# Kernel optimization log

Hardware: AMD Instinct MI355X
Metric: run time of the kernel (lower is better)

Reference implementation:

```python
import jax, jax.numpy as jnp
import numpy as np

V, D, T, B, MS, WIN, EOS = 10000, 256, 128, 8, 4, 1, 4
S = MS + 1          # decoder segment length (y_input0 + MAX_SEGMENT tokens)
HRATE = 0.1
LOGINF = 1e6


def setup_inputs() -> dict:
    key = jax.random.key(0)
    ks = jax.random.split(key, 17)
    s = lambda i, shape: (jax.random.normal(ks[i], shape, jnp.float32) * 0.05)
    return dict(
        x_ids=jax.random.randint(ks[0], (B, T + 2 * WIN), 0, V),
        lens=jnp.full((B,), T, dtype=jnp.int32),
        emb=s(1, (V, D)),
        y_start=s(2, (1, D)),
        cell_Wi=s(3, (4 * D, D)), cell_Wh=s(4, (4 * D, D)), cell_b=s(5, (4 * D,)),
        yin0_W=s(6, (D, D)), yin0_b=s(7, (D,)),
        hlin_W=s(8, (2 * D, D)), hlin_b=s(9, (2 * D,)),
        l0_Wi=s(10, (4 * D, D)), l0_Wh=s(11, (4 * D, D)), l0_b=s(12, (4 * D,)),
        l1_Wi=s(13, (4 * D, D)), l1_Wh=s(14, (4 * D, D)), l1_b=s(15, (4 * D,)),
        out_b=s(16, (V,)),
    )


def _cell(x, h, c, Wi, Wh, b):
    # torch LSTM gate order: i, f, g, o
    g = x @ Wi.T + h @ Wh.T + b
    i, f, gg, o = jnp.split(g, 4, axis=-1)
    c2 = jax.nn.sigmoid(f) * c + jax.nn.sigmoid(i) * jnp.tanh(gg)
    return jax.nn.sigmoid(o) * jnp.tanh(c2), c2


def reference(x_ids, lens, emb, y_start, cell_Wi, cell_Wh, cell_b,
              yin0_W, yin0_b, hlin_W, hlin_b,
              l0_Wi, l0_Wh, l0_b, l1_Wi, l1_Wh, l1_b, out_b):
    y = x_ids[:, WIN:-WIN]                     # [B, T] target ids
    x = emb[y]                                 # [B, T, D]

    # --- encoder LSTMCell scan over j_start (state persists across schedule) ---
    seq = jnp.concatenate(
        [jnp.broadcast_to(y_start, (B, D))[None], jnp.transpose(x, (1, 0, 2))[:-1]], 0)  # [T,B,D]
    z = jnp.zeros((B, D), x.dtype)
    def enc_step(carry, xt):
        h, c = carry
        h2, c2 = _cell(xt, h, c, cell_Wi, cell_Wh, cell_b)
        return (h2, c2), h2
    _, h_seq = jax.lax.scan(enc_step, (z, z), seq)        # [T, B, D]

    drop_h = HRATE * h_seq
    y_in0 = drop_h @ yin0_W.T + yin0_b                    # [T, B, D]
    h0_all = jnp.tanh(drop_h @ hlin_W.T + hlin_b).reshape(T, B, 2, D)  # per-layer init h

    # --- build decoder inputs [T, B, S, D]: (y_input0, x[j_start:j_start+MS]) ---
    xp = jnp.pad(x, ((0, 0), (0, MS), (0, 0)))            # zero-pad time (causal => pads don't affect valid outputs)
    pos = jnp.arange(T)[:, None] + jnp.arange(MS)[None, :]           # [T, MS]
    seg_x = jnp.transpose(xp[:, pos], (1, 0, 2, 3))       # [T, B, MS, D]
    seg = jnp.concatenate([y_in0[:, :, None, :], seg_x], axis=2)     # [T, B, S, D]

    # --- 2-layer LSTM decoder, vmapped over j_start ---
    def decode(seg_t, h_init):                            # seg_t [B,S,D], h_init [B,2,D]
        def step(carry, xt):
            (h0, c0), (h1, c1) = carry
            h0n, c0n = _cell(xt, h0, c0, l0_Wi, l0_Wh, l0_b)
            h1n, c1n = _cell(h0n, h1, c1, l1_Wi, l1_Wh, l1_b)
            return ((h0n, c0n), (h1n, c1n)), h1n
        init = ((h_init[:, 0], z), (h_init[:, 1], z))
        _, hs = jax.lax.scan(step, init, jnp.transpose(seg_t, (1, 0, 2)))
        return jnp.transpose(hs, (1, 0, 2))               # [B, S, D]
    dec_h = jax.vmap(decode)(seg, h0_all)                 # [T, B, S, D]

    # --- tied output projection + log-softmax (only needed gathers kept) ---
    logits = jnp.einsum('tbsd,vd->tbsv', dec_h, emb) + out_b         # [T,B,S,V]
    logZ = jax.nn.logsumexp(logits, axis=-1)                          # [T,B,S]

    tgt = jnp.transpose(y[:, jnp.clip(pos, 0, T - 1)], (1, 0, 2))     # [T,B,MS]
    tgt_lp = jnp.take_along_axis(logits[:, :, :MS, :], tgt[..., None], axis=3)[..., 0] \
             - logZ[:, :, :MS]                                        # [T,B,MS]
    pmask = (pos < T)[:, None, :]
    cum = jnp.cumsum(jnp.where(pmask, tgt_lp, 0.0), axis=2)           # [T,B,MS]
    eos_lp = logits[:, :, 1:, EOS] - logZ[:, :, 1:]                   # [T,B,MS]

    kmask = (jnp.arange(T)[:, None] + jnp.arange(1, MS + 1)[None, :]) <= T   # [T,MS]
    body = jnp.where(kmask[:, None, :], cum + eos_lp, -LOGINF)        # [T,B,MS]
    logpy = jnp.concatenate([jnp.full((T, 1, B), -LOGINF, body.dtype),
                             jnp.transpose(body, (0, 2, 1))], axis=1)  # [T, MS+1, B]

    # --- alpha forward DP: alpha[j] = logsumexp_L alpha[j-L] + logpy[j-L][L] ---
    jj = jnp.arange(1, T + 1)[:, None]
    ii = jnp.arange(MS)[None, :]
    sstart = jj - MS + ii                                             # [T,MS]
    LPG = jnp.where((sstart >= 0)[..., None],
                    logpy[jnp.clip(sstart, 0), jnp.broadcast_to(MS - ii, (T, MS))],
                    -LOGINF)                                          # [T,MS,B]

    Apad0 = jnp.full((MS + T + 1, B), -LOGINF, logpy.dtype).at[MS].set(0.0)
    def dp_step(Apad, args):
        j, lpg = args
        win = jax.lax.dynamic_slice(Apad, (j, 0), (MS, B))            # alpha[j-MS .. j-1]
        aj = jax.nn.logsumexp(win + lpg, axis=0)
        return jax.lax.dynamic_update_slice(Apad, aj[None], (MS + j, 0)), None
    Apad, _ = jax.lax.scan(dp_step, Apad0, (jnp.arange(1, T + 1), LPG))
    alpha = Apad[MS:]                                                 # [T+1, B]

    ret = -jnp.sum(alpha[lens, jnp.arange(B)]) / jnp.sum(lens).astype(alpha.dtype)
    return ret
```

## Files before the change

kernel.cpp:

```cpp
#include <hip/hip_runtime.h>

#define V_ 10000
#define D_ 256
#define T_ 128
#define B_ 8
#define MS_ 4
#define S_ 5
#define EOS_ 4

typedef unsigned short b16_t;
typedef __attribute__((ext_vector_type(8))) short s16x8;
typedef __attribute__((ext_vector_type(8))) unsigned short u16x8;
typedef __attribute__((ext_vector_type(4))) float f32x4;
typedef __attribute__((ext_vector_type(2))) _Float16 h16x2;

__device__ inline b16_t f2bf(float f) {
  union { float f; unsigned u; } v; v.f = f;
  unsigned r = v.u + 0x7FFFu + ((v.u >> 16) & 1u);
  return (b16_t)(r >> 16);
}
__device__ inline float bf2f(b16_t h) {
  union { unsigned u; float f; } v; v.u = ((unsigned)h) << 16; return v.f;
}
__device__ inline float sigm_(float x) { return 1.0f / (1.0f + __expf(-x)); }
__device__ inline float tanh_(float x) { return 2.0f / (1.0f + __expf(-2.0f * x)) - 1.0f; }
__device__ inline h16x2 bch(unsigned u) { return __builtin_bit_cast(h16x2, u); }
__device__ inline unsigned pkh(float a, float b) {
  h16x2 v; v.x = (_Float16)a; v.y = (_Float16)b;
  return __builtin_bit_cast(unsigned, v);
}

#if __has_builtin(__builtin_amdgcn_fdot2)
#define FDOT2(a, b, c) __builtin_amdgcn_fdot2((a), (b), (c), false)
#else
#define FDOT2(a, b, c) ((c) + (float)(a).x * (float)(b).x + (float)(a).y * (float)(b).y)
#endif

__device__ inline float qswap1(float x) {
  return __builtin_bit_cast(float, __builtin_amdgcn_update_dpp(
      0, __builtin_bit_cast(int, x), 0xB1, 0xF, 0xF, true));
}
__device__ inline float qswap2(float x) {
  return __builtin_bit_cast(float, __builtin_amdgcn_update_dpp(
      0, __builtin_bit_cast(int, x), 0x4E, 0xF, 0xF, true));
}

__device__ inline void cvt4(const float* __restrict__ s, b16_t* __restrict__ d) {
  float4 v = *(const float4*)s;
  ushort4 o = { f2bf(v.x), f2bf(v.y), f2bf(v.z), f2bf(v.w) };
  *(ushort4*)d = o;
}

__global__ void k_prep(const float* __restrict__ emb, const float* __restrict__ cWi,
                       const float* __restrict__ y0W, const float* __restrict__ hlW,
                       const float* __restrict__ l0Wi, const float* __restrict__ l0Wh,
                       const float* __restrict__ l1Wi, const float* __restrict__ l1Wh,
                       const float* __restrict__ cWh, const int* __restrict__ x_ids,
                       const float* __restrict__ y_st,
                       b16_t* __restrict__ emb_bf, b16_t* __restrict__ cWi_bf,
                       b16_t* __restrict__ y0W_bf, b16_t* __restrict__ hlW_bf,
                       b16_t* __restrict__ l0Wi_bf, b16_t* __restrict__ l0Wh_bf,
                       b16_t* __restrict__ Wcat_bf, unsigned* __restrict__ Whf,
                       b16_t* __restrict__ seq_bf, b16_t* __restrict__ seg_bf) {
  for (long i = (long)blockIdx.x * blockDim.x + threadIdx.x; i < 1410048L;
       i += (long)gridDim.x * blockDim.x) {
    if (i < 640000L) { cvt4(emb + i * 4, emb_bf + i * 4); }
    else if (i < 705536L) { long j = i - 640000L; cvt4(cWi + j * 4, cWi_bf + j * 4); }
    else if (i < 721920L) { long j = i - 705536L; cvt4(y0W + j * 4, y0W_bf + j * 4); }
    else if (i < 754688L) { long j = i - 721920L; cvt4(hlW + j * 4, hlW_bf + j * 4); }
    else if (i < 820224L) { long j = i - 754688L; cvt4(l0Wi + j * 4, l0Wi_bf + j * 4); }
    else if (i < 885760L) { long j = i - 820224L; cvt4(l0Wh + j * 4, l0Wh_bf + j * 4); }
    else if (i < 1016832L) {
      long j = (i - 885760L) * 4;
      long n = j >> 9; int k = (int)(j & 511);
      const float* src = (k < 256) ? (l1Wi + n * 256 + k) : (l1Wh + n * 256 + (k - 256));
      cvt4(src, Wcat_bf + j);
    } else if (i < 1082368L) {
      long j = i - 1016832L;
      float4 v = *(const float4*)(cWh + j * 4);
      Whf[2 * j] = pkh(v.x, v.y);
      Whf[2 * j + 1] = pkh(v.z, v.w);
    } else if (i < 1147904L) {
      long j = i - 1082368L;
      int m = (int)(j >> 6), c = (int)(j & 63) * 4;
      int t = m >> 3, b = m & 7;
      const float* src = (t == 0) ? (y_st + c)
                                  : (emb + (size_t)x_ids[b * (T_ + 2) + t] * D_ + c);
      cvt4(src, seq_bf + (size_t)m * D_ + c);
    } else {
      long j = i - 1147904L;
      int r = (int)(j >> 6), c = (int)(j & 63) * 4;
      int p = r >> 2, s = 1 + (r & 3);
      int t = p >> 3, b = p & 7;
      int tt = t + s - 1;
      int ps = r + (r >> 2) + 1;
      if (tt < T_) {
        int tok = x_ids[b * (T_ + 2) + tt + 1];
        cvt4(emb + (size_t)tok * D_ + c, seg_bf + (size_t)ps * 256 + c);
      } else {
        ushort4 z = {0, 0, 0, 0};
        *(ushort4*)(seg_bf + (size_t)ps * 256 + c) = z;
      }
    }
  }
}

__global__ __launch_bounds__(256) void k_gemm(const b16_t* __restrict__ A, int lda,
                                              const b16_t* __restrict__ Bw,
                                              const float* __restrict__ bias,
                                              float* __restrict__ C, int ldc) {
  __shared__ b16_t As[64][264];
  __shared__ b16_t Bs[64][264];
  int tid = threadIdx.x;
  int rowBase = blockIdx.x * 64, colBase = blockIdx.y * 64;
  for (int i = tid; i < 64 * 32; i += 256) {
    int r = i >> 5, c = (i & 31) * 8;
    *(u16x8*)&As[r][c] = *(const u16x8*)(A + (size_t)(rowBase + r) * lda + c);
    *(u16x8*)&Bs[r][c] = *(const u16x8*)(Bw + (size_t)(colBase + r) * 256 + c);
  }
  __syncthreads();
  int w = tid >> 6, l = tid & 63, lr = l & 15, kg = l >> 4;
  f32x4 acc[4] = {{0.f,0.f,0.f,0.f},{0.f,0.f,0.f,0.f},{0.f,0.f,0.f,0.f},{0.f,0.f,0.f,0.f}};
  f32x4 acc2[4] = {{0.f,0.f,0.f,0.f},{0.f,0.f,0.f,0.f},{0.f,0.f,0.f,0.f},{0.f,0.f,0.f,0.f}};
  for (int kk = 0; kk < 4; ++kk) {
    s16x8 a = *(const s16x8*)&As[w * 16 + lr][kk * 32 + kg * 8];
    s16x8 a2 = *(const s16x8*)&As[w * 16 + lr][(kk + 4) * 32 + kg * 8];
#pragma unroll
    for (int f = 0; f < 4; ++f) {
      s16x8 b = *(const s16x8*)&Bs[f * 16 + lr][kk * 32 + kg * 8];
      s16x8 b2 = *(const s16x8*)&Bs[f * 16 + lr][(kk + 4) * 32 + kg * 8];
      acc[f] = __builtin_amdgcn_mfma_f32_16x16x32_bf16(a, b, acc[f], 0, 0, 0);
      acc2[f] = __builtin_amdgcn_mfma_f32_16x16x32_bf16(a2, b2, acc2[f], 0, 0, 0);
    }
  }
#pragma unroll
  for (int f = 0; f < 4; ++f) {
#pragma unroll
    for (int r = 0; r < 4; ++r) {
      int m = rowBase + w * 16 + kg * 4 + r;
      int n = colBase + f * 16 + lr;
      C[(size_t)m * ldc + n] = acc[f][r] + acc2[f][r] + bias[n];
    }
  }
}

#define ENC_Q4(i0)                                                             \
  do {                                                                         \
    uint4 a0 = hp[i0], a1 = hp[i0 + 1], a2 = hp[i0 + 2], a3 = hp[i0 + 3];      \
    s0 = FDOT2(bch(a0.x), bch(wv[4 * (i0) + 0]), s0);                          \
    s1 = FDOT2(bch(a0.x), bch(wv[32 + 4 * (i0) + 0]), s1);                     \
    s0 = FDOT2(bch(a0.y), bch(wv[4 * (i0) + 1]), s0);                          \
    s1 = FDOT2(bch(a0.y), bch(wv[32 + 4 * (i0) + 1]), s1);                     \
    s0 = FDOT2(bch(a0.z), bch(wv[4 * (i0) + 2]), s0);                          \
    s1 = FDOT2(bch(a0.z), bch(wv[32 + 4 * (i0) + 2]), s1);                     \
    s0 = FDOT2(bch(a0.w), bch(wv[4 * (i0) + 3]), s0);                          \
    s1 = FDOT2(bch(a0.w), bch(wv[32 + 4 * (i0) + 3]), s1);                     \
    s0 = FDOT2(bch(a1.x), bch(wv[4 * (i0) + 4]), s0);                          \
    s1 = FDOT2(bch(a1.x), bch(wv[32 + 4 * (i0) + 4]), s1);                     \
    s0 = FDOT2(bch(a1.y), bch(wv[4 * (i0) + 5]), s0);                          \
    s1 = FDOT2(bch(a1.y), bch(wv[32 + 4 * (i0) + 5]), s1);                     \
    s0 = FDOT2(bch(a1.z), bch(wv[4 * (i0) + 6]), s0);                          \
    s1 = FDOT2(bch(a1.z), bch(wv[32 + 4 * (i0) + 6]), s1);                     \
    s0 = FDOT2(bch(a1.w), bch(wv[4 * (i0) + 7]), s0);                          \
    s1 = FDOT2(bch(a1.w), bch(wv[32 + 4 * (i0) + 7]), s1);                     \
    s0 = FDOT2(bch(a2.x), bch(wv[4 * (i0) + 8]), s0);                          \
    s1 = FDOT2(bch(a2.x), bch(wv[32 + 4 * (i0) + 8]), s1);                     \
    s0 = FDOT2(bch(a2.y), bch(wv[4 * (i0) + 9]), s0);                          \
    s1 = FDOT2(bch(a2.y), bch(wv[32 + 4 * (i0) + 9]), s1);                     \
    s0 = FDOT2(bch(a2.z), bch(wv[4 * (i0) + 10]), s0);                         \
    s1 = FDOT2(bch(a2.z), bch(wv[32 + 4 * (i0) + 10]), s1);                    \
    s0 = FDOT2(bch(a2.w), bch(wv[4 * (i0) + 11]), s0);                         \
    s1 = FDOT2(bch(a2.w), bch(wv[32 + 4 * (i0) + 11]), s1);                    \
    s0 = FDOT2(bch(a3.x), bch(wv[4 * (i0) + 12]), s0);                         \
    s1 = FDOT2(bch(a3.x), bch(wv[32 + 4 * (i0) + 12]), s1);                    \
    s0 = FDOT2(bch(a3.y), bch(wv[4 * (i0) + 13]), s0);                         \
    s1 = FDOT2(bch(a3.y), bch(wv[32 + 4 * (i0) + 13]), s1);                    \
    s0 = FDOT2(bch(a3.z), bch(wv[4 * (i0) + 14]), s0);                         \
    s1 = FDOT2(bch(a3.z), bch(wv[32 + 4 * (i0) + 14]), s1);                    \
    s0 = FDOT2(bch(a3.w), bch(wv[4 * (i0) + 15]), s0);                         \
    s1 = FDOT2(bch(a3.w), bch(wv[32 + 4 * (i0) + 15]), s1);                    \
  } while (0)

struct EncS { unsigned hbuf[144]; float gl[256]; };
struct GemS { b16_t As[64][264]; b16_t Bs[64][264]; };

__global__ __launch_bounds__(512, 2) void k_enc_x0(
    const unsigned* __restrict__ Whf,
    const float* __restrict__ encX,
    unsigned* __restrict__ hglob,
    b16_t* __restrict__ droph,
    const b16_t* __restrict__ seg_bf, const b16_t* __restrict__ l0Wi_bf,
    const float* __restrict__ l0b, float* __restrict__ X0) {
  __shared__ union { EncS e; GemS g; } sm;
  int tid = threadIdx.x;
  if (blockIdx.x < 32) {
    int b = blockIdx.x & 7, q = blockIdx.x >> 3;
    int rp = tid >> 2, cq = tid & 3;
    int r0l = 2 * rp;
    int grow0 = ((r0l >> 6) << 8) + q * 64 + (r0l & 63);
    unsigned wv[64];
    {
      const uint4* wp0 = (const uint4*)(Whf + (size_t)grow0 * 128 + cq * 32);
      const uint4* wp1 = (const uint4*)(Whf + (size_t)(grow0 + 1) * 128 + cq * 32);
#pragma unroll
      for (int i = 0; i < 8; ++i) {
        uint4 v = wp0[i];
        wv[4*i] = v.x; wv[4*i+1] = v.y; wv[4*i+2] = v.z; wv[4*i+3] = v.w;
      }
#pragma unroll
      for (int i = 0; i < 8; ++i) {
        uint4 v = wp1[i];
        wv[32+4*i] = v.x; wv[32+4*i+1] = v.y; wv[32+4*i+2] = v.z; wv[32+4*i+3] = v.w;
      }
    }
#pragma unroll
    for (int i = 0; i < 64; ++i) asm volatile("" : "+v"(wv[i]));
    if (tid < 144) sm.e.hbuf[tid] = 0;
    float c = 0.f;
    float ex = encX[(size_t)b * 1024 + grow0 + (cq & 1)];
    __syncthreads();
#pragma unroll 1
    for (int t = 0; t < 128; ++t) {
      const uint4* hp = (const uint4*)&sm.e.hbuf[cq * 36];
      float s0 = 0.f, s1 = 0.f;
      ENC_Q4(0);
      __builtin_amdgcn_sched_barrier(0);
      ENC_Q4(4);
      s0 += qswap1(s0); s0 += qswap2(s0);
      s1 += qswap1(s1); s1 += qswap2(s1);
      if (cq == 0) sm.e.gl[r0l] = s0 + ex;
      else if (cq == 1) sm.e.gl[r0l + 1] = s1 + ex;
      __syncthreads();
      if (tid < 64) {
        float gi = sm.e.gl[tid], gf = sm.e.gl[64 + tid];
        float gg = sm.e.gl[128 + tid], go = sm.e.gl[192 + tid];
        float c2 = sigm_(gf) * c + sigm_(gi) * tanh_(gg);
        float h2 = sigm_(go) * tanh_(c2);
        c = c2;
        float hnb = qswap1(h2);
        if ((tid & 1) == 0) {
          unsigned pk = pkh(h2, hnb) | 0x00010001u;
          sm.e.hbuf[q * 36 + (tid >> 1)] = pk;
          if (t < 127)
            __hip_atomic_store(&hglob[(((size_t)t * 8 + b) * 4 + q) * 32 + (tid >> 1)],
                               pk, __ATOMIC_RELAXED, __HIP_MEMORY_SCOPE_AGENT);
        }
        droph[((size_t)t * 8 + b) * 256 + q * 64 + tid] = f2bf(0.1f * h2);
      }
      if (t < 127) {
        if (tid >= 64 && tid < 160) {
          int idx = tid - 64;
          int ro = idx >> 5;
          int rq = ro + (ro >= q);
          int dw = idx & 31;
          unsigned* src = &hglob[(((size_t)t * 8 + b) * 4 + rq) * 32 + dw];
          unsigned v;
          do {
            v = __hip_atomic_load(src, __ATOMIC_RELAXED, __HIP_MEMORY_SCOPE_AGENT);
          } while (v == 0u);
          sm.e.hbuf[rq * 36 + dw] = v;
        }
        ex = encX[((size_t)(t + 1) * 8 + b) * 1024 + grow0 + (cq & 1)];
        __syncthreads();
      }
    }
  } else {
    int bx2 = blockIdx.x - 32;
    int rb = (bx2 & 63) * 64;
    int colBase = (bx2 >> 6) * 64;
    if (tid < 256) {
      for (int i = tid; i < 64 * 32; i += 256) {
        int r = i >> 5, cc = (i & 31) * 8;
        int jj = rb + r, ps = jj + (jj >> 2) + 1;
        *(u16x8*)&sm.g.As[r][cc] = *(const u16x8*)(seg_bf + (size_t)ps * 256 + cc);
        *(u16x8*)&sm.g.Bs[r][cc] = *(const u16x8*)(l0Wi_bf + (size_t)(colBase + r) * 256 + cc);
      }
    }
    __syncthreads();
    if (tid < 256) {
      int w = tid >> 6, l = tid & 63, lr = l & 15, kg = l >> 4;
      f32x4 acc[4] = {{0.f,0.f,0.f,0.f},{0.f,0.f,0.f,0.f},{0.f,0.f,0.f,0.f},{0.f,0.f,0.f,0.f}};
      f32x4 acc2[4] = {{0.f,0.f,0.f,0.f},{0.f,0.f,0.f,0.f},{0.f,0.f,0.f,0.f},{0.f,0.f,0.f,0.f}};
      for (int kk = 0; kk < 4; ++kk) {
        s16x8 a = *(const s16x8*)&sm.g.As[w * 16 + lr][kk * 32 + kg * 8];
        s16x8 a2 = *(const s16x8*)&sm.g.As[w * 16 + lr][(kk + 4) * 32 + kg * 8];
#pragma unroll
        for (int f = 0; f < 4; ++f) {
          s16x8 b = *(const s16x8*)&sm.g.Bs[f * 16 + lr][kk * 32 + kg * 8];
          s16x8 b2 = *(const s16x8*)&sm.g.Bs[f * 16 + lr][(kk + 4) * 32 + kg * 8];
          acc[f] = __builtin_amdgcn_mfma_f32_16x16x32_bf16(a, b, acc[f], 0, 0, 0);
          acc2[f] = __builtin_amdgcn_mfma_f32_16x16x32_bf16(a2, b2, acc2[f], 0, 0, 0);
        }
      }
#pragma unroll
      for (int f = 0; f < 4; ++f) {
#pragma unroll
        for (int r = 0; r < 4; ++r) {
          int jj = rb + w * 16 + kg * 4 + r;
          int ps = jj + (jj >> 2) + 1;
          int n = colBase + f * 16 + lr;
          X0[(size_t)ps * 1024 + n] = acc[f][r] + acc2[f][r] + l0b[n];
        }
      }
    }
  }
}

__global__ __launch_bounds__(256) void k_proj(
    const b16_t* __restrict__ droph, const b16_t* __restrict__ y0W_bf,
    const float* __restrict__ y0b, const b16_t* __restrict__ hlW_bf,
    const float* __restrict__ hlb, b16_t* __restrict__ seg_bf,
    b16_t* __restrict__ hcat,
    const b16_t* __restrict__ l0Wi_bf, const float* __restrict__ l0b,
    float* __restrict__ X0) {
  __shared__ b16_t As[64][264];
  __shared__ b16_t Bs[64][264];
  int bx = blockIdx.x, by = blockIdx.y;
  const b16_t* Ab; int lda;
  const b16_t* Bw; const float* bias; int colBase, mode;
  if (by < 4)       { Ab = droph;  lda = 256;  Bw = y0W_bf;  bias = y0b; colBase = by * 64;        mode = 0; }
  else if (by < 12) { Ab = droph;  lda = 256;  Bw = hlW_bf;  bias = hlb; colBase = (by - 4) * 64;  mode = 1; }
  else              { Ab = seg_bf; lda = 1280; Bw = l0Wi_bf; bias = l0b; colBase = (by - 12) * 64; mode = 2; }
  int rowBase = bx * 64;
  int tid = threadIdx.x;
  for (int i = tid; i < 64 * 32; i += 256) {
    int r = i >> 5, c = (i & 31) * 8;
    *(u16x8*)&As[r][c] = *(const u16x8*)(Ab + (size_t)(rowBase + r) * lda + c);
    *(u16x8*)&Bs[r][c] = *(const u16x8*)(Bw + (size_t)(colBase + r) * 256 + c);
  }
  __syncthreads();
  int w = tid >> 6, l = tid & 63, lr = l & 15, kg = l >> 4;
  f32x4 acc[4] = {{0.f,0.f,0.f,0.f},{0.f,0.f,0.f,0.f},{0.f,0.f,0.f,0.f},{0.f,0.f,0.f,0.f}};
  f32x4 acc2[4] = {{0.f,0.f,0.f,0.f},{0.f,0.f,0.f,0.f},{0.f,0.f,0.f,0.f},{0.f,0.f,0.f,0.f}};
  for (int kk = 0; kk < 4; ++kk) {
    s16x8 a = *(const s16x8*)&As[w * 16 + lr][kk * 32 + kg * 8];
    s16x8 a2 = *(const s16x8*)&As[w * 16 + lr][(kk + 4) * 32 + kg * 8];
#pragma unroll
    for (int f = 0; f < 4; ++f) {
      s16x8 b = *(const s16x8*)&Bs[f * 16 + lr][kk * 32 + kg * 8];
      s16x8 b2 = *(const s16x8*)&Bs[f * 16 + lr][(kk + 4) * 32 + kg * 8];
      acc[f] = __builtin_amdgcn_mfma_f32_16x16x32_bf16(a, b, acc[f], 0, 0, 0);
      acc2[f] = __builtin_amdgcn_mfma_f32_16x16x32_bf16(a2, b2, acc2[f], 0, 0, 0);
    }
  }
#pragma unroll
  for (int f = 0; f < 4; ++f) {
#pragma unroll
    for (int r = 0; r < 4; ++r) {
      int m = rowBase + w * 16 + kg * 4 + r;
      int n = colBase + f * 16 + lr;
      float v = acc[f][r] + acc2[f][r] + bias[n];
      if (mode == 0) seg_bf[(size_t)m * 1280 + n] = f2bf(v);
      else if (mode == 1) hcat[(size_t)m * 512 + n] = f2bf(tanh_(v));
      else X0[(size_t)m * 5120 + n] = v;
    }
  }
}

__global__ __launch_bounds__(512) void k_dec2(
    b16_t* __restrict__ hcat,
    const b16_t* __restrict__ l0Wh_bf,
    const b16_t* __restrict__ Wcat_bf,
    const float* __restrict__ X0,
    const float* __restrict__ l1b,
    float* __restrict__ c0, float* __restrict__ c1,
    b16_t* __restrict__ dec_out, int s) {
  __shared__ b16_t A0s[16][264];
  __shared__ b16_t A1s[16][520];
  int tid = threadIdx.x;
  int R0 = blockIdx.x * 16;
  for (int i = tid; i < 16 * 32; i += 512) {
    int r = i >> 5, cc = (i & 31) * 8;
    *(u16x8*)&A0s[r][cc] = *(const u16x8*)(hcat + (size_t)(R0 + r) * 512 + cc);
    *(u16x8*)&A1s[r][256 + cc] = *(const u16x8*)(hcat + (size_t)(R0 + r) * 512 + 256 + cc);
  }
  __syncthreads();
  int w = tid >> 6, l = tid & 63, lr = l & 15, kg = l >> 4;
  {
    s16x8 af[8];
#pragma unroll
    for (int kk = 0; kk < 8; ++kk)
      af[kk] = *(const s16x8*)&A0s[lr][kk * 32 + kg * 8];
    f32x4 acc[4][2];
#pragma unroll
    for (int g = 0; g < 4; ++g)
#pragma unroll
      for (int ct = 0; ct < 2; ++ct) acc[g][ct] = f32x4{0.f, 0.f, 0.f, 0.f};
#pragma unroll
    for (int g = 0; g < 4; ++g)
#pragma unroll
      for (int ct = 0; ct < 2; ++ct) {
        int n = g * 256 + w * 32 + ct * 16 + lr;
        const b16_t* bp = l0Wh_bf + (size_t)n * 256 + kg * 8;
#pragma unroll
        for (int kk = 0; kk < 8; ++kk)
          acc[g][ct] = __builtin_amdgcn_mfma_f32_16x16x32_bf16(
              af[kk], *(const s16x8*)(bp + kk * 32), acc[g][ct], 0, 0, 0);
      }
#pragma unroll
    for (int ct = 0; ct < 2; ++ct)
#pragma unroll
      for (int r = 0; r < 4; ++r) {
        int row = kg * 4 + r, p = R0 + row, d = w * 32 + ct * 16 + lr;
        const float* xp = X0 + ((size_t)p * 5 + s) * 1024;
        float gi = acc[0][ct][r] + xp[d],       gf = acc[1][ct][r] + xp[256 + d];
        float gg = acc[2][ct][r] + xp[512 + d], go = acc[3][ct][r] + xp[768 + d];
        float cc0 = c0[(size_t)p * 256 + d];
        float c2 = sigm_(gf) * cc0 + sigm_(gi) * tanh_(gg);
        float h2 = sigm_(go) * tanh_(c2);
        c0[(size_t)p * 256 + d] = c2;
        b16_t hb = f2bf(h2);
        A1s[row][d] = hb;
        hcat[(size_t)p * 512 + d] = hb;
      }
  }
  __syncthreads();
  {
    s16x8 a1[16];
#pragma unroll
    for (int kk = 0; kk < 16; ++kk)
      a1[kk] = *(const s16x8*)&A1s[lr][kk * 32 + kg * 8];
    f32x4 acc[4][2];
#pragma unroll
    for (int g = 0; g < 4; ++g)
#pragma unroll
      for (int ct = 0; ct < 2; ++ct) acc[g][ct] = f32x4{0.f, 0.f, 0.f, 0.f};
#pragma unroll
    for (int g = 0; g < 4; ++g)
#pragma unroll
      for (int ct = 0; ct < 2; ++ct) {
        int n = g * 256 + w * 32 + ct * 16 + lr;
        const b16_t* bp = Wcat_bf + (size_t)n * 512 + kg * 8;
#pragma unroll
        for (int kk = 0; kk < 16; ++kk)
          acc[g][ct] = __builtin_amdgcn_mfma_f32_16x16x32_bf16(
              a1[kk], *(const s16x8*)(bp + kk * 32), acc[g][ct], 0, 0, 0);
      }
#pragma unroll
    for (int ct = 0; ct < 2; ++ct)
#pragma unroll
      for (int r = 0; r < 4; ++r) {
        int row = kg * 4 + r, p = R0 + row, d = w * 32 + ct * 16 + lr;
        float gi = acc[0][ct][r] + l1b[d],       gf = acc[1][ct][r] + l1b[256 + d];
        float gg = acc[2][ct][r] + l1b[512 + d], go = acc[3][ct][r] + l1b[768 + d];
        float cc1 = c1[(size_t)p * 256 + d];
        float c2 = sigm_(gf) * cc1 + sigm_(gi) * tanh_(gg);
        float h2 = sigm_(go) * tanh_(c2);
        c1[(size_t)p * 256 + d] = c2;
        b16_t hb = f2bf(h2);
        hcat[(size_t)p * 512 + 256 + d] = hb;
        dec_out[((size_t)p * 5 + s) * 256 + d] = hb;
      }
  }
}

__global__ __launch_bounds__(512) void k_logits_ext(
    const b16_t* __restrict__ Abf, const b16_t* __restrict__ emb_bf,
    const float* __restrict__ out_b, float* __restrict__ sumexp,
    const int* __restrict__ x_ids, float* __restrict__ tl,
    float* __restrict__ el) {
  int bid = blockIdx.x;
  int tid = threadIdx.x;
  if (bid < 560) {
    __shared__ b16_t Bs[64][264];
    int rowBase = (bid % 40) * 128;
    int w = tid >> 6, l = tid & 63, lr = l & 15, kg = l >> 4;
    s16x8 af[8];
    {
      const b16_t* arow = Abf + (size_t)(rowBase + w * 16 + lr) * 256;
#pragma unroll
      for (int kk = 0; kk < 8; ++kk) af[kk] = *(const s16x8*)(arow + kk * 32 + kg * 8);
    }
    float runsum[4] = {0.f, 0.f, 0.f, 0.f};
    int t0 = (bid / 40) * 12, t1 = (t0 + 12 < 157) ? (t0 + 12) : 157;
    for (int tile = t0; tile < t1; ++tile) {
      int colBase = tile * 64;
      __syncthreads();
      for (int i = tid; i < 64 * 32; i += 512) {
        int r = i >> 5, cc = (i & 31) * 8;
        int vrow = colBase + r;
        u16x8 bv = {0, 0, 0, 0, 0, 0, 0, 0};
        if (vrow < V_) bv = *(const u16x8*)(emb_bf + (size_t)vrow * D_ + cc);
        *(u16x8*)&Bs[r][cc] = bv;
      }
      __syncthreads();
      f32x4 acc[4] = {{0.f,0.f,0.f,0.f},{0.f,0.f,0.f,0.f},{0.f,0.f,0.f,0.f},{0.f,0.f,0.f,0.f}};
      f32x4 acc2[4] = {{0.f,0.f,0.f,0.f},{0.f,0.f,0.f,0.f},{0.f,0.f,0.f,0.f},{0.f,0.f,0.f,0.f}};
#pragma unroll
      for (int kk = 0; kk < 4; ++kk) {
#pragma unroll
        for (int f = 0; f < 4; ++f) {
          s16x8 b = *(const s16x8*)&Bs[f * 16 + lr][kk * 32 + kg * 8];
          s16x8 b2 = *(const s16x8*)&Bs[f * 16 + lr][(kk + 4) * 32 + kg * 8];
          acc[f] = __builtin_amdgcn_mfma_f32_16x16x32_bf16(af[kk], b, acc[f], 0, 0, 0);
          acc2[f] = __builtin_amdgcn_mfma_f32_16x16x32_bf16(af[kk + 4], b2, acc2[f], 0, 0, 0);
        }
      }
#pragma unroll
      for (int f = 0; f < 4; ++f) {
        int n = colBase + f * 16 + lr;
        if (n < V_) {
          float ob = out_b[n];
#pragma unroll
          for (int r = 0; r < 4; ++r) runsum[r] += __expf(acc[f][r] + acc2[f][r] + ob);
        }
      }
    }
#pragma unroll
    for (int r = 0; r < 4; ++r) {
      float rs = runsum[r];
      rs += __shfl_xor(rs, 1, 64);
      rs += __shfl_xor(rs, 2, 64);
      rs += __shfl_xor(rs, 4, 64);
      rs += __shfl_xor(rs, 8, 64);
      if (lr == 0) atomicAdd(&sumexp[rowBase + w * 16 + kg * 4 + r], rs);
    }
  } else {
    int p = (bid - 560) * 8 + (tid >> 6);
    int lane = tid & 63;
    int t = p >> 3, b = p & 7;
    for (int s = 0; s < S_; ++s) {
      const b16_t* hr = Abf + ((size_t)p * S_ + s) * D_;
      float hv[4];
#pragma unroll
      for (int j = 0; j < 4; ++j) hv[j] = bf2f(hr[lane * 4 + j]);
      if (s < MS_) {
        int pos = t + s; if (pos > T_ - 1) pos = T_ - 1;
        int tok = x_ids[b * (T_ + 2) + pos + 1];
        const b16_t* er = emb_bf + (size_t)tok * D_;
        float ps = 0.f;
#pragma unroll
        for (int j = 0; j < 4; ++j) ps += hv[j] * bf2f(er[lane * 4 + j]);
        for (int m = 1; m < 64; m <<= 1) ps += __shfl_xor(ps, m, 64);
        if (lane == 0) tl[p * MS_ + s] = ps + out_b[tok];
      }
      if (s >= 1) {
        const b16_t* er = emb_bf + (size_t)EOS_ * D_;
        float ps = 0.f;
#pragma unroll
        for (int j = 0; j < 4; ++j) ps += hv[j] * bf2f(er[lane * 4 + j]);
        for (int m = 1; m < 64; m <<= 1) ps += __shfl_xor(ps, m, 64);
        if (lane == 0) el[p * MS_ + (s - 1)] = ps + out_b[EOS_];
      }
    }
  }
}

__global__ __launch_bounds__(256) void k_final(const float* __restrict__ sumexp,
                                               const float* __restrict__ tl,
                                               const float* __restrict__ el,
                                               const int* __restrict__ lens,
                                               float* __restrict__ out) {
  __shared__ float logpy[T_][S_][B_];
  __shared__ float alpha[T_ + 1][B_];
  int tid = threadIdx.x;
  for (int p = tid; p < T_ * B_; p += 256) {
    int t = p >> 3, b = p & 7;
    float lz[S_];
#pragma unroll
    for (int s = 0; s < S_; ++s) lz[s] = __logf(sumexp[p * S_ + s]);
    float cum = 0.f, cums[MS_];
#pragma unroll
    for (int s = 0; s < MS_; ++s) {
      float tlp = tl[p * MS_ + s] - lz[s];
      if (t + s < T_) cum += tlp;
      cums[s] = cum;
    }
#pragma unroll
    for (int k = 1; k <= MS_; ++k) {
      float bv = -1000000.0f;
      if (t + k <= T_) bv = cums[k - 1] + (el[p * MS_ + (k - 1)] - lz[k]);
      logpy[t][k][b] = bv;
    }
  }
  __syncthreads();
  if (tid < B_) {
    int b = tid;
    alpha[0][b] = 0.f;
    for (int j = 1; j <= T_; ++j) {
      float vs[MS_], vmax = -1e30f;
#pragma unroll
      for (int k = 1; k <= MS_; ++k) {
        float vv = -2000000.0f;
        if (j - k >= 0) vv = alpha[j - k][b] + logpy[j - k][k][b];
        vs[k - 1] = vv;
        if (vv > vmax) vmax = vv;
      }
      float ssum = 0.f;
#pragma unroll
      for (int k = 0; k < MS_; ++k) ssum += __expf(vs[k] - vmax);
      alpha[j][b] = vmax + __logf(ssum);
    }
  }
  __syncthreads();
  if (tid == 0) {
    float num = 0.f, den = 0.f;
    for (int b = 0; b < B_; ++b) { num += alpha[lens[b]][b]; den += (float)lens[b]; }
    out[0] = -num / den;
  }
}

extern "C" void kernel_launch(void* const* d_in, const int* in_sizes, int n_in,
                              void* d_out, int out_size, void* d_ws, size_t ws_size,
                              hipStream_t stream) {
  const int* x_ids   = (const int*)d_in[0];
  const int* lens    = (const int*)d_in[1];
  const float* emb   = (const float*)d_in[2];
  const float* y_st  = (const float*)d_in[3];
  const float* cWi   = (const float*)d_in[4];
  const float* cWh   = (const float*)d_in[5];
  const float* cb    = (const float*)d_in[6];
  const float* y0W   = (const float*)d_in[7];
  const float* y0b   = (const float*)d_in[8];
  const float* hlW   = (const float*)d_in[9];
  const float* hlb   = (const float*)d_in[10];
  const float* l0Wi  = (const float*)d_in[11];
  const float* l0Wh  = (const float*)d_in[12];
  const float* l0b   = (const float*)d_in[13];
  const float* l1Wi  = (const float*)d_in[14];
  const float* l1Wh  = (const float*)d_in[15];
  const float* l1b   = (const float*)d_in[16];
  const float* outb  = (const float*)d_in[17];
  float* out = (float*)d_out;
  (void)in_sizes; (void)n_in; (void)out_size; (void)ws_size;

  char* ws = (char*)d_ws;
  size_t cur = 0;
  auto alloc = [&](size_t bytes) { size_t o = cur; cur += (bytes + 255) & ~(size_t)255; return o; };
  b16_t* emb_bf    = (b16_t*)(ws + alloc((size_t)V_ * D_ * 2));
  b16_t* cWi_bf    = (b16_t*)(ws + alloc(1024 * 256 * 2));
  b16_t* y0W_bf    = (b16_t*)(ws + alloc(256 * 256 * 2));
  b16_t* hlW_bf    = (b16_t*)(ws + alloc(512 * 256 * 2));
  b16_t* l0Wi_bf   = (b16_t*)(ws + alloc(1024 * 256 * 2));
  b16_t* l0Wh_bf   = (b16_t*)(ws + alloc(1024 * 256 * 2));
  b16_t* Wcat_bf   = (b16_t*)(ws + alloc(1024 * 512 * 2));
  unsigned* Whf    = (unsigned*)(ws + alloc(1024 * 128 * 4));
  b16_t* seq_bf    = (b16_t*)(ws + alloc(1024 * 256 * 2));
  float* encX      = (float*)(ws + alloc((size_t)1024 * 1024 * 4));
  b16_t* droph_bf  = (b16_t*)(ws + alloc(1024 * 256 * 2));
  b16_t* hcat      = (b16_t*)(ws + alloc(1024 * 512 * 2));
  b16_t* seg_bf    = (b16_t*)(ws + alloc((size_t)5120 * 256 * 2));
  float* X0        = (float*)(ws + alloc((size_t)5120 * 1024 * 4));
  float* c0        = (float*)(ws + alloc((size_t)2 * 1024 * 256 * 4));
  float* c1        = c0 + 1024 * 256;
  b16_t* dec_h_bf  = (b16_t*)(ws + alloc((size_t)5120 * 256 * 2));
  float* sumexp    = (float*)(ws + alloc(5120 * 4));
  unsigned* hglob  = (unsigned*)(ws + alloc((size_t)128 * 8 * 4 * 32 * 4));
  float* tl        = (float*)(ws + alloc(1024 * MS_ * 4));
  float* el        = (float*)(ws + alloc(1024 * MS_ * 4));

  hipMemsetAsync(sumexp, 0, 20480 + 524288, stream);
  hipMemsetAsync(c0, 0, (size_t)2 * 1024 * 256 * 4, stream);

  k_prep<<<1024, 256, 0, stream>>>(emb, cWi, y0W, hlW, l0Wi, l0Wh, l1Wi, l1Wh, cWh,
                                   x_ids, y_st,
                                   emb_bf, cWi_bf, y0W_bf, hlW_bf, l0Wi_bf, l0Wh_bf,
                                   Wcat_bf, Whf, seq_bf, seg_bf);

  k_gemm<<<dim3(16, 16), 256, 0, stream>>>(seq_bf, 256, cWi_bf, cb, encX, 1024);
  k_enc_x0<<<1056, 512, 0, stream>>>(Whf, encX, hglob, droph_bf,
                                     seg_bf, l0Wi_bf, l0b, X0);

  k_proj<<<dim3(16, 28), 256, 0, stream>>>(droph_bf, y0W_bf, y0b, hlW_bf, hlb,
                                           seg_bf, hcat, l0Wi_bf, l0b, X0);

  for (int s = 0; s < S_; ++s)
    k_dec2<<<64, 512, 0, stream>>>(hcat, l0Wh_bf, Wcat_bf, X0, l1b, c0, c1, dec_h_bf, s);

  k_logits_ext<<<688, 512, 0, stream>>>(dec_h_bf, emb_bf, outb, sumexp,
                                        x_ids, tl, el);
  k_final<<<1, 256, 0, stream>>>(sumexp, tl, el, lens, out);
}
```

Baseline: 547.1 us.

## Interleave two batch chains per encoder block to hide cross-block h exchange latency

```diff
diff --git a/kernel.cpp b/kernel.cpp
--- a/kernel.cpp
+++ b/kernel.cpp
@@ -181,7 +181,7 @@
     s1 = FDOT2(bch(a3.w), bch(wv[32 + 4 * (i0) + 15]), s1);                    \
   } while (0)
 
-struct EncS { unsigned hbuf[144]; float gl[256]; };
+struct EncS { unsigned hbufA[144]; unsigned hbufB[144]; float gl[256]; };
 struct GemS { b16_t As[64][264]; b16_t Bs[64][264]; };
 
 __global__ __launch_bounds__(512, 2) void k_enc_x0(
@@ -193,8 +193,9 @@
     const float* __restrict__ l0b, float* __restrict__ X0) {
   __shared__ union { EncS e; GemS g; } sm;
   int tid = threadIdx.x;
-  if (blockIdx.x < 32) {
-    int b = blockIdx.x & 7, q = blockIdx.x >> 3;
+  if (blockIdx.x < 16) {
+    int pair = blockIdx.x & 3, q = blockIdx.x >> 2;
+    int bA = 2 * pair, bB = 2 * pair + 1;
     int rp = tid >> 2, cq = tid & 3;
     int r0l = 2 * rp;
     int grow0 = ((r0l >> 6) << 8) + q * 64 + (r0l & 63);
@@ -215,57 +216,98 @@
     }
 #pragma unroll
     for (int i = 0; i < 64; ++i) asm volatile("" : "+v"(wv[i]));
-    if (tid < 144) sm.e.hbuf[tid] = 0;
-    float c = 0.f;
-    float ex = encX[(size_t)b * 1024 + grow0 + (cq & 1)];
+    if (tid < 144) { sm.e.hbufA[tid] = 0; sm.e.hbufB[tid] = 0; }
+    float cA = 0.f, cB = 0.f;
+    float exA = encX[(size_t)bA * 1024 + grow0 + (cq & 1)];
+    float exB = encX[(size_t)bB * 1024 + grow0 + (cq & 1)];
     __syncthreads();
 #pragma unroll 1
     for (int t = 0; t < 128; ++t) {
-      const uint4* hp = (const uint4*)&sm.e.hbuf[cq * 36];
-      float s0 = 0.f, s1 = 0.f;
-      ENC_Q4(0);
-      __builtin_amdgcn_sched_barrier(0);
-      ENC_Q4(4);
-      s0 += qswap1(s0); s0 += qswap2(s0);
-      s1 += qswap1(s1); s1 += qswap2(s1);
-      if (cq == 0) sm.e.gl[r0l] = s0 + ex;
-      else if (cq == 1) sm.e.gl[r0l + 1] = s1 + ex;
+      {
+        const uint4* hp = (const uint4*)&sm.e.hbufA[cq * 36];
+        float s0 = 0.f, s1 = 0.f;
+        ENC_Q4(0);
+        __builtin_amdgcn_sched_barrier(0);
+        ENC_Q4(4);
+        s0 += qswap1(s0); s0 += qswap2(s0);
+        s1 += qswap1(s1); s1 += qswap2(s1);
+        if (cq == 0) sm.e.gl[r0l] = s0 + exA;
+        else if (cq == 1) sm.e.gl[r0l + 1] = s1 + exA;
+      }
       __syncthreads();
       if (tid < 64) {
         float gi = sm.e.gl[tid], gf = sm.e.gl[64 + tid];
         float gg = sm.e.gl[128 + tid], go = sm.e.gl[192 + tid];
-        float c2 = sigm_(gf) * c + sigm_(gi) * tanh_(gg);
+        float c2 = sigm_(gf) * cA + sigm_(gi) * tanh_(gg);
         float h2 = sigm_(go) * tanh_(c2);
-        c = c2;
+        cA = c2;
         float hnb = qswap1(h2);
         if ((tid & 1) == 0) {
           unsigned pk = pkh(h2, hnb) | 0x00010001u;
-          sm.e.hbuf[q * 36 + (tid >> 1)] = pk;
+          sm.e.hbufA[q * 36 + (tid >> 1)] = pk;
           if (t < 127)
-            __hip_atomic_store(&hglob[(((size_t)t * 8 + b) * 4 + q) * 32 + (tid >> 1)],
+            __hip_atomic_store(&hglob[(((size_t)t * 8 + bA) * 4 + q) * 32 + (tid >> 1)],
                                pk, __ATOMIC_RELAXED, __HIP_MEMORY_SCOPE_AGENT);
         }
-        droph[((size_t)t * 8 + b) * 256 + q * 64 + tid] = f2bf(0.1f * h2);
-      }
-      if (t < 127) {
-        if (tid >= 64 && tid < 160) {
-          int idx = tid - 64;
-          int ro = idx >> 5;
-          int rq = ro + (ro >= q);
-          int dw = idx & 31;
-          unsigned* src = &hglob[(((size_t)t * 8 + b) * 4 + rq) * 32 + dw];
-          unsigned v;
-          do {
-            v = __hip_atomic_load(src, __ATOMIC_RELAXED, __HIP_MEMORY_SCOPE_AGENT);
-          } while (v == 0u);
-          sm.e.hbuf[rq * 36 + dw] = v;
+        droph[((size_t)t * 8 + bA) * 256 + q * 64 + tid] = f2bf(0.1f * h2);
+      } else if (tid < 160 && t > 0) {
+        int idx = tid - 64;
+        int ro = idx >> 5;
+        int rq = ro + (ro >= q);
+        int dw = idx & 31;
+        unsigned* src = &hglob[(((size_t)(t - 1) * 8 + bB) * 4 + rq) * 32 + dw];
+        unsigned v;
+        do {
+          v = __hip_atomic_load(src, __ATOMIC_RELAXED, __HIP_MEMORY_SCOPE_AGENT);
+        } while (v == 0u);
+        sm.e.hbufB[rq * 36 + dw] = v;
+      }
+      if (t < 127) exA = encX[((size_t)(t + 1) * 8 + bA) * 1024 + grow0 + (cq & 1)];
+      __syncthreads();
+      {
+        const uint4* hp = (const uint4*)&sm.e.hbufB[cq * 36];
+        float s0 = 0.f, s1 = 0.f;
+        ENC_Q4(0);
+        __builtin_amdgcn_sched_barrier(0);
+        ENC_Q4(4);
+        s0 += qswap1(s0); s0 += qswap2(s0);
+        s1 += qswap1(s1); s1 += qswap2(s1);
+        if (cq == 0) sm.e.gl[r0l] = s0 + exB;
+        else if (cq == 1) sm.e.gl[r0l + 1] = s1 + exB;
+      }
+      __syncthreads();
+      if (tid < 64) {
+        float gi = sm.e.gl[tid], gf = sm.e.gl[64 + tid];
+        float gg = sm.e.gl[128 + tid], go = sm.e.gl[192 + tid];
+        float c2 = sigm_(gf) * cB + sigm_(gi) * tanh_(gg);
+        float h2 = sigm_(go) * tanh_(c2);
+        cB = c2;
+        float hnb = qswap1(h2);
+        if ((tid & 1) == 0) {
+          unsigned pk = pkh(h2, hnb) | 0x00010001u;
+          sm.e.hbufB[q * 36 + (tid >> 1)] = pk;
+          if (t < 127)
+            __hip_atomic_store(&hglob[(((size_t)t * 8 + bB) * 4 + q) * 32 + (tid >> 1)],
+                               pk, __ATOMIC_RELAXED, __HIP_MEMORY_SCOPE_AGENT);
         }
-        ex = encX[((size_t)(t + 1) * 8 + b) * 1024 + grow0 + (cq & 1)];
-        __syncthreads();
-      }
+        droph[((size_t)t * 8 + bB) * 256 + q * 64 + tid] = f2bf(0.1f * h2);
+      } else if (tid < 160 && t < 127) {
+        int idx = tid - 64;
+        int ro = idx >> 5;
+        int rq = ro + (ro >= q);
+        int dw = idx & 31;
+        unsigned* src = &hglob[(((size_t)t * 8 + bA) * 4 + rq) * 32 + dw];
+        unsigned v;
+        do {
+          v = __hip_atomic_load(src, __ATOMIC_RELAXED, __HIP_MEMORY_SCOPE_AGENT);
+        } while (v == 0u);
+        sm.e.hbufA[rq * 36 + dw] = v;
+      }
+      if (t < 127) exB = encX[((size_t)(t + 1) * 8 + bB) * 1024 + grow0 + (cq & 1)];
+      __syncthreads();
     }
   } else {
-    int bx2 = blockIdx.x - 32;
+    int bx2 = blockIdx.x - 16;
     int rb = (bx2 & 63) * 64;
     int colBase = (bx2 >> 6) * 64;
     if (tid < 256) {
@@ -658,7 +700,7 @@
                                    Wcat_bf, Whf, seq_bf, seg_bf);
 
   k_gemm<<<dim3(16, 16), 256, 0, stream>>>(seq_bf, 256, cWi_bf, cb, encX, 1024);
-  k_enc_x0<<<1056, 512, 0, stream>>>(Whf, encX, hglob, droph_bf,
+  k_enc_x0<<<1040, 512, 0, stream>>>(Whf, encX, hglob, droph_bf,
                                      seg_bf, l0Wi_bf, l0b, X0);
 
   k_proj<<<dim3(16, 28), 256, 0, stream>>>(droph_bf, y0W_bf, y0b, hlW_bf, hlb,
```

New measurement: 592.0 us. +8.2%, slower.
